# Performance work log

Measured on AMD Instinct MI355X. Metric: run time of the kernel, lower is better.

The kernel has to match this reference:

```python
import math
import jax, jax.numpy as jnp
import numpy as np


def setup_inputs() -> dict:
    key = jax.random.key(0)
    k1, k2 = jax.random.split(key)
    B, Sq, Sk, H, Hkv, D = 2, 2048, 2048, 16, 8, 128
    q = jax.random.normal(k1, (B, Sq, H, D), dtype=jnp.float32)
    kv = jax.random.normal(k2, (B, Sk, 2, Hkv, D), dtype=jnp.float32)
    return {"q": q, "kv": kv}


def reference(q, kv):
    # q: [B, Sq, H, D]; kv: [B, Sk, 2, Hkv, D]
    B, Sq, H, D = q.shape
    Sk = kv.shape[1]
    Hkv = kv.shape[3]
    if Hkv != H:
        # GQA: repeat each kv head g times consecutively ('... hkv d -> ... (hkv g) d')
        kv = jnp.repeat(kv, H // Hkv, axis=3)
    k = kv[:, :, 0]  # [B, Sk, H, D]
    v = kv[:, :, 1]  # [B, Sk, H, D]
    q = q.astype(jnp.float32)
    k = k.astype(jnp.float32)
    scale = 1.0 / math.sqrt(D)
    # scores: [B, H, Sq, Sk]
    scores = jnp.einsum('bqhd,bkhd->bhqk', q, k * scale)
    # causal mask with right-alignment offset: mask where col > row + Sk - Sq
    rows = jnp.arange(Sq)[:, None]
    cols = jnp.arange(Sk)[None, :]
    causal_mask = cols > rows + (Sk - Sq)  # [Sq, Sk]
    scores = jnp.where(causal_mask[None, None], jnp.float32(-10000.0), scores)
    attention = jax.nn.softmax(scores, axis=-1).astype(v.dtype)
    # output: [B, Sq, H, D]
    out = jnp.einsum('bhqk,bkhd->bqhd', attention, v)
    return out
```

## Files before the change

### kernel.cpp

```cpp
#include <hip/hip_runtime.h>
#include <stdint.h>


#define SQ 2048
#define SK 2048
#define NH 16
#define NKV 8
#define DH 128
#define KVSTRIDE (2*NKV*DH)
#define SCALE_LOG2E 0.12751743f

typedef __attribute__((ext_vector_type(8))) short bf8;
typedef __attribute__((ext_vector_type(4))) float f4;
typedef __attribute__((ext_vector_type(4))) int i4;

__device__ __forceinline__ float fast_exp2(float x) {
  return __builtin_amdgcn_exp2f(x);
}

__device__ __forceinline__ short f2bf(float f) {
  uint32_t u = __builtin_bit_cast(uint32_t, f);
  u += 0x7FFFu + ((u >> 16) & 1u);
  return (short)(u >> 16);
}

__device__ __forceinline__ int cvtpk(float lo, float hi) {
  int r;
  asm("v_cvt_pk_bf16_f32 %0, %1, %2" : "=v"(r) : "v"(lo), "v"(hi));
  return r;
}

__device__ __forceinline__ bf8 pack8(f4 a, f4 b) {
  bf8 v;
  v[0] = f2bf(a[0]); v[1] = f2bf(a[1]); v[2] = f2bf(a[2]); v[3] = f2bf(a[3]);
  v[4] = f2bf(b[0]); v[5] = f2bf(b[1]); v[6] = f2bf(b[2]); v[7] = f2bf(b[3]);
  return v;
}
__device__ __forceinline__ bf8 pack8s(f4 a, f4 b, float s) {
  bf8 v;
  v[0] = f2bf(a[0]*s); v[1] = f2bf(a[1]*s); v[2] = f2bf(a[2]*s); v[3] = f2bf(a[3]*s);
  v[4] = f2bf(b[0]*s); v[5] = f2bf(b[1]*s); v[6] = f2bf(b[2]*s); v[7] = f2bf(b[3]*s);
  return v;
}

template<int CTRL>
__device__ __forceinline__ float dppmov(float x) {
  int xi = __builtin_bit_cast(int, x);
  int r = __builtin_amdgcn_update_dpp(xi, xi, CTRL, 0xF, 0xF, false);
  return __builtin_bit_cast(float, r);
}
__device__ __forceinline__ float rowsum16(float v) {
  v += dppmov<0x121>(v);
  v += dppmov<0x122>(v);
  v += dppmov<0x124>(v);
  v += dppmov<0x128>(v);
  return v;
}
__device__ __forceinline__ float rowmax16(float v) {
  v = fmaxf(v, dppmov<0x121>(v));
  v = fmaxf(v, dppmov<0x122>(v));
  v = fmaxf(v, dppmov<0x124>(v));
  v = fmaxf(v, dppmov<0x128>(v));
  return v;
}

__device__ __forceinline__ void g2l16(const short* g, short* l) {
  __builtin_amdgcn_global_load_lds(
      (const __attribute__((address_space(1))) uint32_t*)g,
      (__attribute__((address_space(3))) uint32_t*)l, 16, 0, 0);
}

__global__ void conv_kv(const float* __restrict__ kv,
                        short* __restrict__ Kb, short* __restrict__ Vb) {
  int id = blockIdx.x * 256 + threadIdx.x;
  if (blockIdx.y == 0) {
    int c   = id & 15;
    int key = (id >> 4) & 63;
    int kt  = (id >> 10) & 31;
    int hk  = (id >> 15) & 7;
    int b   = (id >> 18) & 1;
    const float* src = kv + ((size_t)(b * SK + kt * 64 + key) * 2) * (NKV * DH)
                          + hk * DH + c * 8;
    f4 a = *(const f4*)src;
    f4 bb = *(const f4*)(src + 4);
    short* dst = Kb + ((size_t)((b * 8 + hk) * 32 + kt)) * 8192;
    int akey = (key & 0x23) | ((key & 4) << 2) | ((key & 0x18) >> 1);
    *(bf8*)&dst[(akey * 16 + (c ^ (akey & 7))) * 8] = pack8(a, bb);
  } else {
    int d  = id & 127;
    int c  = (id >> 7) & 7;
    int kt = (id >> 10) & 31;
    int hk = (id >> 15) & 7;
    int b  = (id >> 18) & 1;
    const float* src = kv + ((size_t)(b * SK + kt * 64 + c * 8) * 2 + 1) * (NKV * DH)
                          + hk * DH + d;
    bf8 v;
#pragma unroll
    for (int kk = 0; kk < 8; ++kk) v[kk] = f2bf(src[(size_t)kk * KVSTRIDE]);
    short* dst = Vb + ((size_t)((b * 8 + hk) * 32 + kt)) * 8192;
    *(bf8*)&dst[(d * 8 + (c ^ (d & 7))) * 8] = v;
  }
}

__launch_bounds__(256, 2)
__global__ void fa_fwd9(const float* __restrict__ q,
                        const short* __restrict__ Kb,
                        const short* __restrict__ Vb,
                        float* __restrict__ out) {
  __shared__ __align__(16) short lsKV[4][8192];
  __shared__ __align__(16) float lsL[256];

  const int tid  = threadIdx.x;
  const int w    = tid >> 6;
  const int l    = tid & 63;
  const int l15  = l & 15;
  const int quad = l >> 4;

  const int bx   = blockIdx.x;
  const int p    = bx >> 5;
  const int rem  = bx & 31;
  const int b    = rem >> 4;
  const int head = rem & 15;
  const int hk   = head >> 1;

  const int h     = w >> 1;
  const int mrow0 = (w & 1) * 32;

  const short* ktiles = Kb + ((size_t)((b * 8 + hk) * 32)) * 8192;
  const short* vtiles = Vb + ((size_t)((b * 8 + hk) * 32)) * 8192;

  auto stage = [&](int kt, int nb) {
    const short* ks = ktiles + (size_t)kt * 8192 + tid * 8;
    const short* vs = vtiles + (size_t)kt * 8192 + tid * 8;
#pragma unroll
    for (int i = 0; i < 4; ++i) {
      g2l16(ks + i * 2048, &lsKV[nb][i * 2048 + tid * 8]);
      g2l16(vs + i * 2048, &lsKV[2 + nb][i * 2048 + tid * 8]);
    }
  };

#pragma unroll 1
  for (int phase = 0; phase < 2; ++phase) {
    const int qt = phase ? (31 - p) : p;
    const int q0 = qt * 64;

    bf8 qf[2][4];
#pragma unroll
    for (int mt = 0; mt < 2; ++mt) {
      int row = q0 + mrow0 + mt * 16 + l15;
      const float* qr = q + ((size_t)(b * SQ + row) * NH + head) * DH;
#pragma unroll
      for (int kc = 0; kc < 4; ++kc) {
        const float* src = qr + kc * 32 + quad * 8;
        f4 a = *(const f4*)src;
        f4 c = *(const f4*)(src + 4);
        qf[mt][kc] = pack8s(a, c, SCALE_LOG2E);
      }
    }

    f4 O[2][8];
#pragma unroll
    for (int mt = 0; mt < 2; ++mt)
#pragma unroll
      for (int nt = 0; nt < 8; ++nt) O[mt][nt] = (f4){0.f, 0.f, 0.f, 0.f};
    float lpart[2] = {0.f, 0.f};

    if (phase) __syncthreads();
    stage(0, 0);

    for (int kt = 0; kt <= qt; ++kt) {
      const int cur = kt & 1;
      __syncthreads();
      if (kt < qt) stage(kt + 1, cur ^ 1);

      f4 S[2][2];
#pragma unroll
      for (int mt = 0; mt < 2; ++mt)
#pragma unroll
        for (int nt = 0; nt < 2; ++nt) S[mt][nt] = (f4){0.f, 0.f, 0.f, 0.f};
      __builtin_amdgcn_s_setprio(1);
#pragma unroll
      for (int kc = 0; kc < 4; ++kc) {
#pragma unroll
        for (int nt = 0; nt < 2; ++nt) {
          int row = h * 32 + nt * 16 + l15;
          int c   = kc * 4 + quad;
          bf8 kf = *(const bf8*)&lsKV[cur][(row * 16 + (c ^ (row & 7))) * 8];
          S[0][nt] = __builtin_amdgcn_mfma_f32_16x16x32_bf16(kf, qf[0][kc], S[0][nt], 0, 0, 0);
          S[1][nt] = __builtin_amdgcn_mfma_f32_16x16x32_bf16(kf, qf[1][kc], S[1][nt], 0, 0, 0);
        }
      }
      __builtin_amdgcn_s_setprio(0);

      if (kt == qt) {
#pragma unroll
        for (int mt = 0; mt < 2; ++mt)
#pragma unroll
          for (int nt = 0; nt < 2; ++nt)
#pragma unroll
            for (int r = 0; r < 4; ++r) {
              int kphys = h * 32 + (quad << 3) + (nt << 2) + r;
              if (kphys > mrow0 + mt * 16 + l15) S[mt][nt][r] = -1e30f;
            }
      }

#pragma unroll
      for (int mt = 0; mt < 2; ++mt)
#pragma unroll
        for (int nt = 0; nt < 2; ++nt)
#pragma unroll
          for (int r = 0; r < 4; ++r) {
            float pe = fast_exp2(S[mt][nt][r]);
            S[mt][nt][r] = pe;
            lpart[mt] += pe;
          }

      bf8 pf[2];
#pragma unroll
      for (int mt = 0; mt < 2; ++mt) {
        i4 wv;
        wv[0] = cvtpk(S[mt][0][0], S[mt][0][1]);
        wv[1] = cvtpk(S[mt][0][2], S[mt][0][3]);
        wv[2] = cvtpk(S[mt][1][0], S[mt][1][1]);
        wv[3] = cvtpk(S[mt][1][2], S[mt][1][3]);
        pf[mt] = __builtin_bit_cast(bf8, wv);
      }

      __builtin_amdgcn_s_setprio(1);
#pragma unroll
      for (int nt = 0; nt < 8; ++nt) {
        int d = nt * 16 + l15;
        int c = h * 4 + quad;
        bf8 vf = *(const bf8*)&lsKV[2 + cur][(d * 8 + (c ^ (d & 7))) * 8];
        O[0][nt] = __builtin_amdgcn_mfma_f32_16x16x32_bf16(pf[0], vf, O[0][nt], 0, 0, 0);
        O[1][nt] = __builtin_amdgcn_mfma_f32_16x16x32_bf16(pf[1], vf, O[1][nt], 0, 0, 0);
      }
      __builtin_amdgcn_s_setprio(0);
    }

    __syncthreads();
    if (w >= 2) {
      int uw = w - 2;
      float* base = (float*)lsKV[uw] + (size_t)l * 64;
#pragma unroll
      for (int mt = 0; mt < 2; ++mt)
#pragma unroll
        for (int nt = 0; nt < 8; ++nt) {
          int tt   = mt * 8 + nt;
          int slot = (tt + l15) & 15;
          *(f4*)(base + slot * 4) = O[mt][nt];
        }
      lsL[(uw * 64 + l) * 2 + 0] = lpart[0];
      lsL[(uw * 64 + l) * 2 + 1] = lpart[1];
    }
    __syncthreads();
    if (w < 2) {
      float* base = (float*)lsKV[w] + (size_t)l * 64;
#pragma unroll
      for (int mt = 0; mt < 2; ++mt)
#pragma unroll
        for (int nt = 0; nt < 8; ++nt) {
          int tt   = mt * 8 + nt;
          int slot = (tt + l15) & 15;
          O[mt][nt] += *(const f4*)(base + slot * 4);
        }
      lpart[0] += lsL[(w * 64 + l) * 2 + 0];
      lpart[1] += lsL[(w * 64 + l) * 2 + 1];

#pragma unroll
      for (int mt = 0; mt < 2; ++mt) {
        float lsum = lpart[mt];
        lsum += __shfl_xor(lsum, 16);
        lsum += __shfl_xor(lsum, 32);
#pragma unroll
        for (int r = 0; r < 4; ++r) {
          float lr   = __shfl(lsum, quad * 4 + r);
          float linv = 1.0f / lr;
          int row = q0 + mrow0 + mt * 16 + quad * 4 + r;
          float* dst = out + ((size_t)(b * SQ + row) * NH + head) * DH + l15;
#pragma unroll
          for (int nt = 0; nt < 8; ++nt) dst[nt * 16] = O[mt][nt][r] * linv;
        }
      }
    }
  }
}

__launch_bounds__(256, 2)
__global__ void fa_fwd_v1(const float* __restrict__ q,
                          const float* __restrict__ kv,
                          float* __restrict__ out) {
  __shared__ __align__(16) short lsK[64 * 128];
  __shared__ __align__(16) short lsV[128 * 64];
  __shared__ __align__(16) short lsP[4][32 * 64];

  const int tid  = threadIdx.x;
  const int w    = tid >> 6;
  const int l    = tid & 63;
  const int l15  = l & 15;
  const int quad = l >> 4;

  const int bx  = blockIdx.x;
  const int qt  = 31 - (bx >> 4);
  const int bhk = bx & 15;
  const int b   = bhk >> 3;
  const int hk  = bhk & 7;
  const int head  = hk * 2 + (w >> 1);
  const int mrow0 = (w & 1) * 32;
  const int q0    = qt * 64;

  const float* kbase = kv + (size_t)b * SK * KVSTRIDE + (size_t)hk * DH;
  const float* vbase = kbase + NKV * DH;

  bf8 qf[2][4];
#pragma unroll
  for (int mt = 0; mt < 2; ++mt)
#pragma unroll
    for (int kc = 0; kc < 4; ++kc) {
      int row = q0 + mrow0 + mt * 16 + l15;
      int d0  = kc * 32 + quad * 8;
      const float* src = q + ((size_t)(b * SQ + row) * NH + head) * DH + d0;
      f4 a = *(const f4*)src;
      f4 c = *(const f4*)(src + 4);
      qf[mt][kc] = pack8s(a, c, SCALE_LOG2E);
    }

  f4 O[2][8];
  float mrow[2][4], lrow[2][4];
#pragma unroll
  for (int mt = 0; mt < 2; ++mt) {
#pragma unroll
    for (int nt = 0; nt < 8; ++nt) O[mt][nt] = (f4){0.f, 0.f, 0.f, 0.f};
#pragma unroll
    for (int r = 0; r < 4; ++r) { mrow[mt][r] = -1e30f; lrow[mt][r] = 0.f; }
  }

  for (int kt = 0; kt <= qt; ++kt) {
    if (kt) __syncthreads();
    const int k0 = kt * 64;
#pragma unroll
    for (int i = 0; i < 4; ++i) {
      int id  = i * 256 + tid;
      int key = id >> 4;
      int c   = id & 15;
      const float* src = kbase + (size_t)(k0 + key) * KVSTRIDE + c * 8;
      f4 a = *(const f4*)src;
      f4 bb = *(const f4*)(src + 4);
      *(bf8*)&lsK[(key * 16 + (c ^ (key & 7))) * 8] = pack8(a, bb);
    }
#pragma unroll
    for (int i = 0; i < 4; ++i) {
      int u  = i * 4 + w;
      int kg = u >> 1;
      int d  = (u & 1) * 64 + l;
      const float* src = vbase + (size_t)(k0 + kg * 8) * KVSTRIDE + d;
      bf8 v;
#pragma unroll
      for (int kk = 0; kk < 8; ++kk) v[kk] = f2bf(src[(size_t)kk * KVSTRIDE]);
      *(bf8*)&lsV[(d * 8 + (kg ^ (d & 7))) * 8] = v;
    }
    __syncthreads();

    f4 S[2][4];
#pragma unroll
    for (int mt = 0; mt < 2; ++mt)
#pragma unroll
      for (int nt = 0; nt < 4; ++nt) S[mt][nt] = (f4){0.f, 0.f, 0.f, 0.f};
#pragma unroll
    for (int kc = 0; kc < 4; ++kc)
#pragma unroll
      for (int nt = 0; nt < 4; ++nt) {
        int key = nt * 16 + l15;
        int c   = kc * 4 + quad;
        bf8 kf = *(const bf8*)&lsK[(key * 16 + (c ^ (key & 7))) * 8];
        S[0][nt] = __builtin_amdgcn_mfma_f32_16x16x32_bf16(qf[0][kc], kf, S[0][nt], 0, 0, 0);
        S[1][nt] = __builtin_amdgcn_mfma_f32_16x16x32_bf16(qf[1][kc], kf, S[1][nt], 0, 0, 0);
      }

    if (kt == qt) {
#pragma unroll
      for (int mt = 0; mt < 2; ++mt)
#pragma unroll
        for (int nt = 0; nt < 4; ++nt)
#pragma unroll
          for (int r = 0; r < 4; ++r) {
            int rloc = mrow0 + mt * 16 + quad * 4 + r;
            int kloc = nt * 16 + l15;
            if (kloc > rloc) S[mt][nt][r] = -1e30f;
          }
    }

#pragma unroll
    for (int mt = 0; mt < 2; ++mt)
#pragma unroll
      for (int r = 0; r < 4; ++r) {
        float mx = fmaxf(fmaxf(S[mt][0][r], S[mt][1][r]),
                         fmaxf(S[mt][2][r], S[mt][3][r]));
        mx = rowmax16(mx);
        float mold = mrow[mt][r];
        float mnew = fmaxf(mold, mx);
        float alpha = fast_exp2(mold - mnew);
        mrow[mt][r] = mnew;
        float rs = 0.f;
#pragma unroll
        for (int nt = 0; nt < 4; ++nt) {
          float pe = fast_exp2(S[mt][nt][r] - mnew);
          S[mt][nt][r] = pe;
          rs += pe;
        }
        rs = rowsum16(rs);
        lrow[mt][r] = lrow[mt][r] * alpha + rs;
#pragma unroll
        for (int nt = 0; nt < 8; ++nt) O[mt][nt][r] *= alpha;
        int m = mt * 16 + quad * 4 + r;
#pragma unroll
        for (int nt = 0; nt < 4; ++nt) {
          int key = nt * 16 + l15;
          lsP[w][(m * 8 + ((key >> 3) ^ (m & 7))) * 8 + (key & 7)] =
              f2bf(S[mt][nt][r]);
        }
      }

#pragma unroll
    for (int kc = 0; kc < 2; ++kc) {
      bf8 pf[2];
#pragma unroll
      for (int mt = 0; mt < 2; ++mt) {
        int m = mt * 16 + l15;
        int c = kc * 4 + quad;
        pf[mt] = *(const bf8*)&lsP[w][(m * 8 + (c ^ (m & 7))) * 8];
      }
#pragma unroll
      for (int nt = 0; nt < 8; ++nt) {
        int d = nt * 16 + l15;
        int c = kc * 4 + quad;
        bf8 vf = *(const bf8*)&lsV[(d * 8 + (c ^ (d & 7))) * 8];
        O[0][nt] = __builtin_amdgcn_mfma_f32_16x16x32_bf16(pf[0], vf, O[0][nt], 0, 0, 0);
        O[1][nt] = __builtin_amdgcn_mfma_f32_16x16x32_bf16(pf[1], vf, O[1][nt], 0, 0, 0);
      }
    }
  }

#pragma unroll
  for (int mt = 0; mt < 2; ++mt)
#pragma unroll
    for (int r = 0; r < 4; ++r) {
      float linv = 1.0f / lrow[mt][r];
      int row = q0 + mrow0 + mt * 16 + quad * 4 + r;
      float* dst = out + ((size_t)(b * SQ + row) * NH + head) * DH + l15;
#pragma unroll
      for (int nt = 0; nt < 8; ++nt) dst[nt * 16] = O[mt][nt][r] * linv;
    }
}

extern "C" void kernel_launch(void* const* d_in, const int* in_sizes, int n_in,
                              void* d_out, int out_size, void* d_ws, size_t ws_size,
                              hipStream_t stream) {
  const float* q  = (const float*)d_in[0];
  const float* kv = (const float*)d_in[1];
  float* out      = (float*)d_out;
  (void)in_sizes; (void)n_in; (void)out_size;

  const size_t kb_elems = (size_t)2 * 8 * 32 * 8192;
  const size_t need = 2 * kb_elems * sizeof(short);

  if (ws_size >= need) {
    short* Kb = (short*)d_ws;
    short* Vb = Kb + kb_elems;
    conv_kv<<<dim3(2048, 2), 256, 0, stream>>>(kv, Kb, Vb);
    fa_fwd9<<<dim3(512), dim3(256), 0, stream>>>(q, Kb, Vb, out);
  } else {
    fa_fwd_v1<<<dim3(512), dim3(256), 0, stream>>>(q, kv, out);
  }
}
```

Baseline: 147.7 us.

## Load K/V fragments directly from global into registers, dropping LDS staging

Removes the double-buffered LDS staging of K and V tiles and the per-iteration block barrier. Each wave now reads its own K and V MFMA fragments straight from global memory. K fragments for the next tile are prefetched into registers during the current iteration, and V fragments are loaded at the start of each iteration. LDS is kept only for the final cross-wave output reduction. The aim is to cut barrier stalls and LDS traffic. In exchange, the two waves that share a head-half both fetch the same fragments, which doubles cache traffic, and the register prefetch buffers raise register pressure.

```diff
diff --git a/kernel.cpp b/kernel.cpp
--- a/kernel.cpp
+++ b/kernel.cpp
@@ -62,12 +62,6 @@
   v = fmaxf(v, dppmov<0x124>(v));
   v = fmaxf(v, dppmov<0x128>(v));
   return v;
-}
-
-__device__ __forceinline__ void g2l16(const short* g, short* l) {
-  __builtin_amdgcn_global_load_lds(
-      (const __attribute__((address_space(1))) uint32_t*)g,
-      (__attribute__((address_space(3))) uint32_t*)l, 16, 0, 0);
 }
 
 __global__ void conv_kv(const float* __restrict__ kv,
@@ -103,12 +97,12 @@
 }
 
 __launch_bounds__(256, 2)
-__global__ void fa_fwd9(const float* __restrict__ q,
-                        const short* __restrict__ Kb,
-                        const short* __restrict__ Vb,
-                        float* __restrict__ out) {
-  __shared__ __align__(16) short lsKV[4][8192];
-  __shared__ __align__(16) float lsL[256];
+__global__ void fa_fwd10(const float* __restrict__ q,
+                         const short* __restrict__ Kb,
+                         const short* __restrict__ Vb,
+                         float* __restrict__ out) {
+  __shared__ __align__(16) float lsO[2][4096];
+  __shared__ float lsL[256];
 
   const int tid  = threadIdx.x;
   const int w    = tid >> 6;
@@ -129,16 +123,6 @@
   const short* ktiles = Kb + ((size_t)((b * 8 + hk) * 32)) * 8192;
   const short* vtiles = Vb + ((size_t)((b * 8 + hk) * 32)) * 8192;
 
-  auto stage = [&](int kt, int nb) {
-    const short* ks = ktiles + (size_t)kt * 8192 + tid * 8;
-    const short* vs = vtiles + (size_t)kt * 8192 + tid * 8;
-#pragma unroll
-    for (int i = 0; i < 4; ++i) {
-      g2l16(ks + i * 2048, &lsKV[nb][i * 2048 + tid * 8]);
-      g2l16(vs + i * 2048, &lsKV[2 + nb][i * 2048 + tid * 8]);
-    }
-  };
-
 #pragma unroll 1
   for (int phase = 0; phase < 2; ++phase) {
     const int qt = phase ? (31 - p) : p;
@@ -165,13 +149,26 @@
       for (int nt = 0; nt < 8; ++nt) O[mt][nt] = (f4){0.f, 0.f, 0.f, 0.f};
     float lpart[2] = {0.f, 0.f};
 
-    if (phase) __syncthreads();
-    stage(0, 0);
-
+    bf8 kpre[4][2];
+#pragma unroll
+    for (int kc = 0; kc < 4; ++kc)
+#pragma unroll
+      for (int nt = 0; nt < 2; ++nt) {
+        int row = h * 32 + nt * 16 + l15;
+        int c   = kc * 4 + quad;
+        kpre[kc][nt] = *(const bf8*)&ktiles[(row * 16 + (c ^ (row & 7))) * 8];
+      }
+
+#pragma unroll 1
     for (int kt = 0; kt <= qt; ++kt) {
-      const int cur = kt & 1;
-      __syncthreads();
-      if (kt < qt) stage(kt + 1, cur ^ 1);
+      const short* vt = vtiles + (size_t)kt * 8192;
+      bf8 vf[8];
+#pragma unroll
+      for (int nt = 0; nt < 8; ++nt) {
+        int d = nt * 16 + l15;
+        int c = h * 4 + quad;
+        vf[nt] = *(const bf8*)&vt[(d * 8 + (c ^ (d & 7))) * 8];
+      }
 
       f4 S[2][2];
 #pragma unroll
@@ -183,14 +180,23 @@
       for (int kc = 0; kc < 4; ++kc) {
 #pragma unroll
         for (int nt = 0; nt < 2; ++nt) {
-          int row = h * 32 + nt * 16 + l15;
-          int c   = kc * 4 + quad;
-          bf8 kf = *(const bf8*)&lsKV[cur][(row * 16 + (c ^ (row & 7))) * 8];
-          S[0][nt] = __builtin_amdgcn_mfma_f32_16x16x32_bf16(kf, qf[0][kc], S[0][nt], 0, 0, 0);
-          S[1][nt] = __builtin_amdgcn_mfma_f32_16x16x32_bf16(kf, qf[1][kc], S[1][nt], 0, 0, 0);
+          S[0][nt] = __builtin_amdgcn_mfma_f32_16x16x32_bf16(kpre[kc][nt], qf[0][kc], S[0][nt], 0, 0, 0);
+          S[1][nt] = __builtin_amdgcn_mfma_f32_16x16x32_bf16(kpre[kc][nt], qf[1][kc], S[1][nt], 0, 0, 0);
         }
       }
       __builtin_amdgcn_s_setprio(0);
+
+      if (kt < qt) {
+        const short* kt1 = ktiles + (size_t)(kt + 1) * 8192;
+#pragma unroll
+        for (int kc = 0; kc < 4; ++kc)
+#pragma unroll
+          for (int nt = 0; nt < 2; ++nt) {
+            int row = h * 32 + nt * 16 + l15;
+            int c   = kc * 4 + quad;
+            kpre[kc][nt] = *(const bf8*)&kt1[(row * 16 + (c ^ (row & 7))) * 8];
+          }
+      }
 
       if (kt == qt) {
 #pragma unroll
@@ -229,11 +235,8 @@
       __builtin_amdgcn_s_setprio(1);
 #pragma unroll
       for (int nt = 0; nt < 8; ++nt) {
-        int d = nt * 16 + l15;
-        int c = h * 4 + quad;
-        bf8 vf = *(const bf8*)&lsKV[2 + cur][(d * 8 + (c ^ (d & 7))) * 8];
-        O[0][nt] = __builtin_amdgcn_mfma_f32_16x16x32_bf16(pf[0], vf, O[0][nt], 0, 0, 0);
-        O[1][nt] = __builtin_amdgcn_mfma_f32_16x16x32_bf16(pf[1], vf, O[1][nt], 0, 0, 0);
+        O[0][nt] = __builtin_amdgcn_mfma_f32_16x16x32_bf16(pf[0], vf[nt], O[0][nt], 0, 0, 0);
+        O[1][nt] = __builtin_amdgcn_mfma_f32_16x16x32_bf16(pf[1], vf[nt], O[1][nt], 0, 0, 0);
       }
       __builtin_amdgcn_s_setprio(0);
     }
@@ -241,7 +244,7 @@
     __syncthreads();
     if (w >= 2) {
       int uw = w - 2;
-      float* base = (float*)lsKV[uw] + (size_t)l * 64;
+      float* base = lsO[uw] + (size_t)l * 64;
 #pragma unroll
       for (int mt = 0; mt < 2; ++mt)
 #pragma unroll
@@ -255,7 +258,7 @@
     }
     __syncthreads();
     if (w < 2) {
-      float* base = (float*)lsKV[w] + (size_t)l * 64;
+      float* base = lsO[w] + (size_t)l * 64;
 #pragma unroll
       for (int mt = 0; mt < 2; ++mt)
 #pragma unroll
@@ -468,7 +471,7 @@
     short* Kb = (short*)d_ws;
     short* Vb = Kb + kb_elems;
     conv_kv<<<dim3(2048, 2), 256, 0, stream>>>(kv, Kb, Vb);
-    fa_fwd9<<<dim3(512), dim3(256), 0, stream>>>(q, Kb, Vb, out);
+    fa_fwd10<<<dim3(512), dim3(256), 0, stream>>>(q, Kb, Vb, out);
   } else {
     fa_fwd_v1<<<dim3(512), dim3(256), 0, stream>>>(q, kv, out);
   }
```

New measurement: 172.4 us. +16.7%, slower.

## Share KV tiles across both GQA heads in 512-thread blocks with 128-key steps

Applied to the files above, without the earlier changes.

Each block now handles both query heads that share one KV head, so each K/V tile staged into LDS serves two heads instead of being loaded twice. The kernel also processes two 64-key tiles per iteration, with the two wave halves splitting the key tiles, and fully masks any out-of-range half tile. This halves KV global traffic and the number of barriers. The cost is 512-thread blocks at one block per CU, a grid that shrinks from 512 to 256 blocks, and some wasted work on masked half tiles.

```diff
diff --git a/kernel.cpp b/kernel.cpp
--- a/kernel.cpp
+++ b/kernel.cpp
@@ -102,13 +102,14 @@
   }
 }
 
-__launch_bounds__(256, 2)
-__global__ void fa_fwd9(const float* __restrict__ q,
-                        const short* __restrict__ Kb,
-                        const short* __restrict__ Vb,
-                        float* __restrict__ out) {
-  __shared__ __align__(16) short lsKV[4][8192];
-  __shared__ __align__(16) float lsL[256];
+__launch_bounds__(512, 1)
+__global__ void fa_fwd12(const float* __restrict__ q,
+                         const short* __restrict__ Kb,
+                         const short* __restrict__ Vb,
+                         float* __restrict__ out) {
+  __shared__ __align__(16) short lsA[2][16384];
+  __shared__ __align__(16) short lsB[2][16384];
+  __shared__ float lsL[512];
 
   const int tid  = threadIdx.x;
   const int w    = tid >> 6;
@@ -116,26 +117,26 @@
   const int l15  = l & 15;
   const int quad = l >> 4;
 
-  const int bx   = blockIdx.x;
-  const int p    = bx >> 5;
-  const int rem  = bx & 31;
-  const int b    = rem >> 4;
-  const int head = rem & 15;
-  const int hk   = head >> 1;
-
-  const int h     = w >> 1;
-  const int mrow0 = (w & 1) * 32;
+  const int bx  = blockIdx.x;
+  const int p   = bx >> 4;
+  const int bhk = bx & 15;
+  const int b   = bhk >> 3;
+  const int hk  = bhk & 7;
+
+  const int h     = w >> 2;
+  const int head  = hk * 2 + (w & 1);
+  const int mrow0 = ((w >> 1) & 1) * 32;
 
   const short* ktiles = Kb + ((size_t)((b * 8 + hk) * 32)) * 8192;
   const short* vtiles = Vb + ((size_t)((b * 8 + hk) * 32)) * 8192;
 
-  auto stage = [&](int kt, int nb) {
-    const short* ks = ktiles + (size_t)kt * 8192 + tid * 8;
-    const short* vs = vtiles + (size_t)kt * 8192 + tid * 8;
+  auto stage = [&](int T, int nb) {
+    const short* ks = ktiles + (size_t)(2 * T) * 8192 + tid * 8;
+    const short* vs = vtiles + (size_t)(2 * T) * 8192 + tid * 8;
 #pragma unroll
     for (int i = 0; i < 4; ++i) {
-      g2l16(ks + i * 2048, &lsKV[nb][i * 2048 + tid * 8]);
-      g2l16(vs + i * 2048, &lsKV[2 + nb][i * 2048 + tid * 8]);
+      g2l16(ks + i * 4096, &lsA[nb][i * 4096 + tid * 8]);
+      g2l16(vs + i * 4096, &lsB[nb][i * 4096 + tid * 8]);
     }
   };
 
@@ -143,6 +144,7 @@
   for (int phase = 0; phase < 2; ++phase) {
     const int qt = phase ? (31 - p) : p;
     const int q0 = qt * 64;
+    const int NT = qt >> 1;
 
     bf8 qf[2][4];
 #pragma unroll
@@ -168,46 +170,60 @@
     if (phase) __syncthreads();
     stage(0, 0);
 
-    for (int kt = 0; kt <= qt; ++kt) {
-      const int cur = kt & 1;
+#pragma unroll 1
+    for (int T = 0; T <= NT; ++T) {
+      const int cur = T & 1;
       __syncthreads();
-      if (kt < qt) stage(kt + 1, cur ^ 1);
-
-      f4 S[2][2];
-#pragma unroll
-      for (int mt = 0; mt < 2; ++mt)
-#pragma unroll
-        for (int nt = 0; nt < 2; ++nt) S[mt][nt] = (f4){0.f, 0.f, 0.f, 0.f};
+      if (T < NT) stage(T + 1, cur ^ 1);
+
+      const short* Kc = &lsA[cur][h * 8192];
+      const short* Vc = &lsB[cur][h * 8192];
+
+      f4 S[2][4];
+#pragma unroll
+      for (int mt = 0; mt < 2; ++mt)
+#pragma unroll
+        for (int nt = 0; nt < 4; ++nt) S[mt][nt] = (f4){0.f, 0.f, 0.f, 0.f};
       __builtin_amdgcn_s_setprio(1);
 #pragma unroll
       for (int kc = 0; kc < 4; ++kc) {
 #pragma unroll
-        for (int nt = 0; nt < 2; ++nt) {
-          int row = h * 32 + nt * 16 + l15;
+        for (int nt = 0; nt < 4; ++nt) {
+          int row = nt * 16 + l15;
           int c   = kc * 4 + quad;
-          bf8 kf = *(const bf8*)&lsKV[cur][(row * 16 + (c ^ (row & 7))) * 8];
+          bf8 kf = *(const bf8*)&Kc[(row * 16 + (c ^ (row & 7))) * 8];
           S[0][nt] = __builtin_amdgcn_mfma_f32_16x16x32_bf16(kf, qf[0][kc], S[0][nt], 0, 0, 0);
           S[1][nt] = __builtin_amdgcn_mfma_f32_16x16x32_bf16(kf, qf[1][kc], S[1][nt], 0, 0, 0);
         }
       }
       __builtin_amdgcn_s_setprio(0);
 
-      if (kt == qt) {
-#pragma unroll
-        for (int mt = 0; mt < 2; ++mt)
-#pragma unroll
-          for (int nt = 0; nt < 2; ++nt)
-#pragma unroll
-            for (int r = 0; r < 4; ++r) {
-              int kphys = h * 32 + (quad << 3) + (nt << 2) + r;
-              if (kphys > mrow0 + mt * 16 + l15) S[mt][nt][r] = -1e30f;
-            }
-      }
-
-#pragma unroll
-      for (int mt = 0; mt < 2; ++mt)
-#pragma unroll
-        for (int nt = 0; nt < 2; ++nt)
+      const int st = 2 * T + h;
+      if (st >= qt) {
+        if (st > qt) {
+#pragma unroll
+          for (int mt = 0; mt < 2; ++mt)
+#pragma unroll
+            for (int nt = 0; nt < 4; ++nt)
+#pragma unroll
+              for (int r = 0; r < 4; ++r) S[mt][nt][r] = -1e30f;
+        } else {
+#pragma unroll
+          for (int mt = 0; mt < 2; ++mt)
+#pragma unroll
+            for (int nt = 0; nt < 4; ++nt)
+#pragma unroll
+              for (int r = 0; r < 4; ++r) {
+                int kphys = ((nt >> 1) << 5) + (quad << 3) + ((nt & 1) << 2) + r;
+                if (kphys > mrow0 + mt * 16 + l15) S[mt][nt][r] = -1e30f;
+              }
+        }
+      }
+
+#pragma unroll
+      for (int mt = 0; mt < 2; ++mt)
+#pragma unroll
+        for (int nt = 0; nt < 4; ++nt)
 #pragma unroll
           for (int r = 0; r < 4; ++r) {
             float pe = fast_exp2(S[mt][nt][r]);
@@ -215,33 +231,38 @@
             lpart[mt] += pe;
           }
 
-      bf8 pf[2];
-#pragma unroll
-      for (int mt = 0; mt < 2; ++mt) {
-        i4 wv;
-        wv[0] = cvtpk(S[mt][0][0], S[mt][0][1]);
-        wv[1] = cvtpk(S[mt][0][2], S[mt][0][3]);
-        wv[2] = cvtpk(S[mt][1][0], S[mt][1][1]);
-        wv[3] = cvtpk(S[mt][1][2], S[mt][1][3]);
-        pf[mt] = __builtin_bit_cast(bf8, wv);
-      }
+      bf8 pf[2][2];
+#pragma unroll
+      for (int mt = 0; mt < 2; ++mt)
+#pragma unroll
+        for (int kc2 = 0; kc2 < 2; ++kc2) {
+          i4 wv;
+          wv[0] = cvtpk(S[mt][2*kc2][0],   S[mt][2*kc2][1]);
+          wv[1] = cvtpk(S[mt][2*kc2][2],   S[mt][2*kc2][3]);
+          wv[2] = cvtpk(S[mt][2*kc2+1][0], S[mt][2*kc2+1][1]);
+          wv[3] = cvtpk(S[mt][2*kc2+1][2], S[mt][2*kc2+1][3]);
+          pf[mt][kc2] = __builtin_bit_cast(bf8, wv);
+        }
 
       __builtin_amdgcn_s_setprio(1);
 #pragma unroll
-      for (int nt = 0; nt < 8; ++nt) {
-        int d = nt * 16 + l15;
-        int c = h * 4 + quad;
-        bf8 vf = *(const bf8*)&lsKV[2 + cur][(d * 8 + (c ^ (d & 7))) * 8];
-        O[0][nt] = __builtin_amdgcn_mfma_f32_16x16x32_bf16(pf[0], vf, O[0][nt], 0, 0, 0);
-        O[1][nt] = __builtin_amdgcn_mfma_f32_16x16x32_bf16(pf[1], vf, O[1][nt], 0, 0, 0);
+      for (int kc2 = 0; kc2 < 2; ++kc2) {
+#pragma unroll
+        for (int nt = 0; nt < 8; ++nt) {
+          int d = nt * 16 + l15;
+          int c = kc2 * 4 + quad;
+          bf8 vf = *(const bf8*)&Vc[(d * 8 + (c ^ (d & 7))) * 8];
+          O[0][nt] = __builtin_amdgcn_mfma_f32_16x16x32_bf16(pf[0][kc2], vf, O[0][nt], 0, 0, 0);
+          O[1][nt] = __builtin_amdgcn_mfma_f32_16x16x32_bf16(pf[1][kc2], vf, O[1][nt], 0, 0, 0);
+        }
       }
       __builtin_amdgcn_s_setprio(0);
     }
 
     __syncthreads();
-    if (w >= 2) {
-      int uw = w - 2;
-      float* base = (float*)lsKV[uw] + (size_t)l * 64;
+    if (w >= 4) {
+      int uw = w - 4;
+      float* base = (float*)&lsA[0][0] + uw * 4096 + (size_t)l * 64;
 #pragma unroll
       for (int mt = 0; mt < 2; ++mt)
 #pragma unroll
@@ -254,8 +275,8 @@
       lsL[(uw * 64 + l) * 2 + 1] = lpart[1];
     }
     __syncthreads();
-    if (w < 2) {
-      float* base = (float*)lsKV[w] + (size_t)l * 64;
+    if (w < 4) {
+      float* base = (float*)&lsA[0][0] + w * 4096 + (size_t)l * 64;
 #pragma unroll
       for (int mt = 0; mt < 2; ++mt)
 #pragma unroll
@@ -468,7 +489,7 @@
     short* Kb = (short*)d_ws;
     short* Vb = Kb + kb_elems;
     conv_kv<<<dim3(2048, 2), 256, 0, stream>>>(kv, Kb, Vb);
-    fa_fwd9<<<dim3(512), dim3(256), 0, stream>>>(q, Kb, Vb, out);
+    fa_fwd12<<<dim3(256), dim3(512), 0, stream>>>(q, Kb, Vb, out);
   } else {
     fa_fwd_v1<<<dim3(512), dim3(256), 0, stream>>>(q, kv, out);
   }
```

Result: no change. 147.4 us (-0.2%).
